# Performance work log

Hardware: AMD Instinct MI355X
Metric: run time of the kernel (lower is better)

The kernel has to match this reference:

```python
import jax, jax.numpy as jnp
import numpy as np

S, N, H, AD, AR = 256, 1024, 512, 128, 2

def setup_inputs() -> dict:
    key = jax.random.key(0)
    k0, k1, k2, k3, k4, k5 = jax.random.split(key, 6)
    xav1 = np.sqrt(2.0 / (H + AD)).astype(np.float32)   # xavier_normal std for [H,AD]
    xav2 = np.sqrt(2.0 / (AD + AR)).astype(np.float32)  # xavier_normal std for [AD,AR]
    return {
        "pre_emb_padded": jax.random.normal(k0, (S, N, H), jnp.float32),
        "fol_emb_padded": jax.random.normal(k1, (S, N, H), jnp.float32),
        "pre_attn_mask": jnp.zeros((N, S), jnp.bool_),
        "fol_attn_mask": jnp.zeros((N, S), jnp.bool_),
        "pre_is_valid": jnp.ones((N,), jnp.int32),
        "fol_is_valid": jnp.ones((N,), jnp.int32),
        "W1_pre": jax.random.normal(k2, (H, AD), jnp.float32) * xav1,
        "W2_pre": jax.random.normal(k3, (AD, AR), jnp.float32) * xav2,
        "W1_fol": jax.random.normal(k4, (H, AD), jnp.float32) * xav1,
        "W2_fol": jax.random.normal(k5, (AD, AR), jnp.float32) * xav2,
    }

def _attn_pool(emb, mask, W1, W2):
    # emb: [S, N, H] -> x: [N, S, H]
    x = jnp.transpose(emb, (1, 0, 2))
    s = jnp.tanh(x @ W1) @ W2                 # [N, S, 2]
    s = jax.nn.softmax(s, axis=1)             # softmax over seq (first softmax)
    s = jnp.transpose(s, (0, 2, 1))           # [N, 2, S]
    s = jnp.where(mask[:, None, :], -jnp.inf, s)
    s = jax.nn.softmax(s, axis=-1)            # masked second softmax over seq
    return jnp.einsum('nrs,nsh->nrh', s, x)   # [N, 2, H]

def _scatter_valid(h, valid):
    # reproduce the python valid-list gather: valid rows take next chunk, else zeros
    pos = jnp.cumsum(valid) - 1               # [N]
    return jnp.where((valid > 0)[:, None, None], h[pos], jnp.zeros((), h.dtype))

def reference(pre_emb_padded, fol_emb_padded, pre_attn_mask, fol_attn_mask,
              pre_is_valid, fol_is_valid, W1_pre, W2_pre, W1_fol, W2_fol):
    h_pre = _scatter_valid(_attn_pool(pre_emb_padded, pre_attn_mask, W1_pre, W2_pre), pre_is_valid)
    h_fol = _scatter_valid(_attn_pool(fol_emb_padded, fol_attn_mask, W1_fol, W2_fol), fol_is_valid)
    # mean over the attn_r=2 rows, concat along feature dim -> [N, 1, 2H]
    return jnp.concatenate([h_pre.mean(axis=1, keepdims=True),
                            h_fol.mean(axis=1, keepdims=True)], axis=2)
```

## Files before the change

### kernel.cpp

```cpp
#include <hip/hip_runtime.h>
#include <hip/hip_bf16.h>
#include <cstdint>
#include <cstddef>

#define S_ 256
#define N_ 1024
#define H_ 512
#define AD_ 128
static constexpr int M_TOTAL = N_ * S_;

typedef __attribute__((ext_vector_type(8))) short short8;
typedef __attribute__((ext_vector_type(4))) float f32x4;

__global__ __launch_bounds__(256) void k_w1frag(
    const float* __restrict__ w1_pre, const float* __restrict__ w1_fol,
    unsigned short* __restrict__ w1f) {
  int idx = blockIdx.x * 256 + threadIdx.x;
  int st = blockIdx.y;
  const float* w1 = st ? w1_fol : w1_pre;
  int j = idx & 7;
  int lane = (idx >> 3) & 63;
  int c = (idx >> 9) & 7;
  int kk = idx >> 12;
  int k = kk * 32 + ((lane >> 4) << 3) + j;
  int d = c * 16 + (lane & 15);
  __hip_bfloat16 hb = __float2bfloat16(w1[(size_t)k * AD_ + d]);
  w1f[(size_t)st * 65536 + idx] = *(unsigned short*)&hb;
}

__global__ __launch_bounds__(1024) void k_scan(
    const int* __restrict__ valid_pre, const int* __restrict__ valid_fol,
    int* __restrict__ pos) {
  const int st = blockIdx.x;
  const int* valid = st ? valid_fol : valid_pre;
  __shared__ int buf[1024];
  const int t = threadIdx.x;
  buf[t] = valid[t];
  __syncthreads();
  for (int off = 1; off < 1024; off <<= 1) {
    int v = (t >= off) ? buf[t - off] : 0;
    __syncthreads();
    buf[t] += v;
    __syncthreads();
  }
  pos[st * N_ + t] = buf[t] - 1;
}

__global__ __launch_bounds__(512) void k_logits(
    const float* __restrict__ emb_pre, const float* __restrict__ emb_fol,
    const unsigned short* __restrict__ w1f,
    const float* __restrict__ w2_pre, const float* __restrict__ w2_fol,
    float* __restrict__ logits) {
  __shared__ __align__(16) unsigned char As[16384];
  __shared__ float part[8][16][2];

  const int bid = blockIdx.x;
  const int st  = bid >> 7;
  const int idx = bid & 127;
  const int nc  = idx >> 1;
  const int sh  = idx & 1;
  const int n0 = nc * 16, s0 = sh * 128;
  const float* __restrict__ emb = st ? emb_fol : emb_pre;
  const float* __restrict__ w2  = st ? w2_fol : w2_pre;

  const int t = threadIdx.x;
  const int w = t >> 6, lane = t & 63;
  const int r16 = lane & 15, kq = lane >> 4;

  short8 B[16];
  {
    const unsigned short* bb = w1f + (size_t)st * 65536 + w * 512 + (size_t)lane * 8;
#pragma unroll
    for (int kk = 0; kk < 16; ++kk) B[kk] = *(const short8*)(bb + kk * 4096);
  }
  const float w2v0 = w2[(w * 16 + r16) * 2 + 0];
  const float w2v1 = w2[(w * 16 + r16) * 2 + 1];

  const int srow = t >> 5;
  const int sl   = t & 31;
  const size_t SSTR = (size_t)N_ * H_;
  const float* sbase = emb + ((size_t)s0 * N_ + n0 + srow) * H_ + sl * 4;
  unsigned wadr[4];
#pragma unroll
  for (int j = 0; j < 4; ++j) {
    int g = j * 16 + (sl >> 1);
    wadr[j] = (unsigned)(srow * 1024 + ((g ^ (srow & 7)) * 16) + (sl & 1) * 8);
  }
  unsigned radr[16];
#pragma unroll
  for (int kk = 0; kk < 16; ++kk)
    radr[kk] = (unsigned)(r16 * 1024 + (((kk * 4 + kq) ^ (r16 & 7)) * 16));

  float4 nxt[4];
#pragma unroll
  for (int j = 0; j < 4; ++j) nxt[j] = *(const float4*)(sbase + j * 128);
#pragma unroll
  for (int j = 0; j < 4; ++j) {
    union { unsigned long long u; __hip_bfloat162 h[2]; } p;
    p.h[0] = __float22bfloat162_rn(make_float2(nxt[j].x, nxt[j].y));
    p.h[1] = __float22bfloat162_rn(make_float2(nxt[j].z, nxt[j].w));
    *(unsigned long long*)&As[wadr[j]] = p.u;
  }
  __syncthreads();

  for (int ss = 0; ss < 128; ++ss) {
    if (ss < 127) {
      const float* nb = sbase + (size_t)(ss + 1) * SSTR;
#pragma unroll
      for (int j = 0; j < 4; ++j) nxt[j] = *(const float4*)(nb + j * 128);
    }

    f32x4 acc = (f32x4){0.f, 0.f, 0.f, 0.f};
#pragma unroll
    for (int kk = 0; kk < 16; ++kk) {
      short8 a = *(const short8*)&As[radr[kk]];
      acc = __builtin_amdgcn_mfma_f32_16x16x32_bf16(a, B[kk], acc, 0, 0, 0);
    }

#pragma unroll
    for (int q = 0; q < 4; ++q) {
      float xc = fminf(fmaxf(acc[q], -10.f), 10.f);
      float e  = __expf(2.f * xc);
      float th = (e - 1.f) / (e + 1.f);
      float p0 = th * w2v0;
      float p1 = th * w2v1;
      p0 += __shfl_xor(p0, 1); p0 += __shfl_xor(p0, 2);
      p0 += __shfl_xor(p0, 4); p0 += __shfl_xor(p0, 8);
      p1 += __shfl_xor(p1, 1); p1 += __shfl_xor(p1, 2);
      p1 += __shfl_xor(p1, 4); p1 += __shfl_xor(p1, 8);
      if (r16 == 0) {
        part[w][kq * 4 + q][0] = p0;
        part[w][kq * 4 + q][1] = p1;
      }
    }
    __syncthreads();

    if (t < 32) {
      int row = t >> 1, rr = t & 1;
      float v = 0.f;
#pragma unroll
      for (int g = 0; g < 8; ++g) v += part[g][row][rr];
      logits[((size_t)st * M_TOTAL + (size_t)(s0 + ss) * N_ + n0 + row) * 2 + rr] = v;
    }
    if (ss < 127) {
#pragma unroll
      for (int j = 0; j < 4; ++j) {
        union { unsigned long long u; __hip_bfloat162 h[2]; } p;
        p.h[0] = __float22bfloat162_rn(make_float2(nxt[j].x, nxt[j].y));
        p.h[1] = __float22bfloat162_rn(make_float2(nxt[j].z, nxt[j].w));
        *(unsigned long long*)&As[wadr[j]] = p.u;
      }
    }
    __syncthreads();
  }
}

template <bool MAXRED>
__device__ __forceinline__ float blockRed(float v, float* buf) {
#pragma unroll
  for (int off = 32; off; off >>= 1) {
    float o = __shfl_xor(v, off);
    v = MAXRED ? fmaxf(v, o) : (v + o);
  }
  __syncthreads();
  if ((threadIdx.x & 63) == 0) buf[threadIdx.x >> 6] = v;
  __syncthreads();
  float r = buf[0];
#pragma unroll
  for (int i = 1; i < 4; ++i) r = MAXRED ? fmaxf(r, buf[i]) : (r + buf[i]);
  return r;
}

__global__ __launch_bounds__(256) void k_softmax(
    const float* __restrict__ logits,
    const unsigned char* __restrict__ mask_pre, const unsigned char* __restrict__ mask_fol,
    float* __restrict__ wbar) {
  const int n  = blockIdx.x;
  const int st = blockIdx.y;
  const unsigned char* mask = st ? mask_fol : mask_pre;
  const int s = threadIdx.x;

  float2 l = *(const float2*)&logits[((size_t)st * M_TOTAL + (size_t)s * N_ + n) * 2];
  const bool mk = mask[(size_t)n * S_ + s] != 0;

  __shared__ float buf[4];
  float q[2];
  float lv[2] = {l.x, l.y};
#pragma unroll
  for (int r = 0; r < 2; ++r) {
    float m1 = blockRed<true>(lv[r], buf);
    float e1 = __expf(lv[r] - m1);
    float s1 = blockRed<false>(e1, buf);
    float p1 = e1 / s1;
    float v  = mk ? -INFINITY : p1;
    float m2 = blockRed<true>(v, buf);
    float e2 = mk ? 0.f : __expf(v - m2);
    float s2 = blockRed<false>(e2, buf);
    q[r] = e2 / s2;
  }
  wbar[((size_t)st * N_ + n) * S_ + s] = 0.5f * (q[0] + q[1]);
}

__global__ __launch_bounds__(512) void k_pv2(
    const float* __restrict__ emb_pre, const float* __restrict__ emb_fol,
    const float* __restrict__ wbar,
    float* __restrict__ part) {
  const int bid = blockIdx.x;
  const int st  = bid >> 7;
  const int idx = bid & 127;
  const int nc  = idx >> 1;
  const int sh  = idx & 1;
  const int n0 = nc * 16, s0 = sh * 128;
  const float* __restrict__ emb = st ? emb_fol : emb_pre;

  const int t = threadIdx.x;
  const int nl = t >> 5;
  const int c0 = (t & 31) * 4;

  __shared__ float wl[16][128];
  for (int i = t; i < 2048; i += 512) {
    int j = i >> 7, sl = i & 127;
    wl[j][sl] = wbar[((size_t)st * N_ + n0 + j) * S_ + s0 + sl];
  }
  __syncthreads();

  float4 acc[4], cur[4], nxt[4];
#pragma unroll
  for (int j = 0; j < 4; ++j) acc[j] = (float4){0.f, 0.f, 0.f, 0.f};

  const float* rowp = emb + ((size_t)(s0 + 127) * N_ + n0 + nl) * H_ + c0;
  const size_t SSTR = (size_t)N_ * H_;
#pragma unroll
  for (int j = 0; j < 4; ++j) cur[j] = *(const float4*)(rowp + j * 128);

  for (int sl = 127; sl >= 0; --sl) {
    const float* nrow = rowp - SSTR;
    if (sl > 0) {
#pragma unroll
      for (int j = 0; j < 4; ++j) nxt[j] = *(const float4*)(nrow + j * 128);
    }
    const float wv = wl[nl][sl];
#pragma unroll
    for (int j = 0; j < 4; ++j) {
      acc[j].x += wv * cur[j].x;
      acc[j].y += wv * cur[j].y;
      acc[j].z += wv * cur[j].z;
      acc[j].w += wv * cur[j].w;
    }
#pragma unroll
    for (int j = 0; j < 4; ++j) cur[j] = nxt[j];
    rowp = nrow;
  }

  float* pp = part + (((size_t)(st * 2 + sh) * N_) + n0 + nl) * H_ + c0;
#pragma unroll
  for (int j = 0; j < 4; ++j) *(float4*)(pp + j * 128) = acc[j];
}

__global__ __launch_bounds__(256) void k_combine(
    const float* __restrict__ part, const int* __restrict__ pos,
    const int* __restrict__ valid_pre, const int* __restrict__ valid_fol,
    float* __restrict__ out) {
  const int n = blockIdx.x, t = threadIdx.x;
  const int st = t >> 7;
  const int c = (t & 127) * 4;
  const int* valid = st ? valid_fol : valid_pre;
  float4 r = {0.f, 0.f, 0.f, 0.f};
  if (valid[n] > 0) {
    int np = pos[st * N_ + n]; if (np < 0) np = 0;
    float4 a = *(const float4*)&part[(((size_t)(st * 2 + 0) * N_) + np) * H_ + c];
    float4 b = *(const float4*)&part[(((size_t)(st * 2 + 1) * N_) + np) * H_ + c];
    r.x = a.x + b.x; r.y = a.y + b.y; r.z = a.z + b.z; r.w = a.w + b.w;
  }
  *(float4*)&out[(size_t)n * 1024 + st * 512 + c] = r;
}

extern "C" void kernel_launch(void* const* d_in, const int* in_sizes, int n_in,
                              void* d_out, int out_size, void* d_ws, size_t ws_size,
                              hipStream_t stream) {
  const float* emb_pre = (const float*)d_in[0];
  const float* emb_fol = (const float*)d_in[1];
  const unsigned char* mask_pre = (const unsigned char*)d_in[2];
  const unsigned char* mask_fol = (const unsigned char*)d_in[3];
  const int* valid_pre = (const int*)d_in[4];
  const int* valid_fol = (const int*)d_in[5];
  const float* w1_pre = (const float*)d_in[6];
  const float* w2_pre = (const float*)d_in[7];
  const float* w1_fol = (const float*)d_in[8];
  const float* w2_fol = (const float*)d_in[9];
  float* out = (float*)d_out;

  char* ws = (char*)d_ws;
  unsigned short* w1f = (unsigned short*)ws;
  int*   pos    = (int*)(ws + 262144);
  float* logits = (float*)(ws + 270336);
  float* wbar   = (float*)(ws + 270336 + 4194304);
  float* part   = (float*)(ws + 270336 + 4194304 + 2097152);

  hipLaunchKernelGGL(k_w1frag, dim3(256, 2), dim3(256), 0, stream,
                     w1_pre, w1_fol, w1f);
  hipLaunchKernelGGL(k_scan, dim3(2), dim3(1024), 0, stream,
                     valid_pre, valid_fol, pos);
  hipLaunchKernelGGL(k_logits, dim3(256), dim3(512), 0, stream,
                     emb_pre, emb_fol, w1f, w2_pre, w2_fol, logits);
  hipLaunchKernelGGL(k_softmax, dim3(N_, 2), dim3(256), 0, stream,
                     logits, mask_pre, mask_fol, wbar);
  hipLaunchKernelGGL(k_pv2, dim3(256), dim3(512), 0, stream,
                     emb_pre, emb_fol, wbar, part);
  hipLaunchKernelGGL(k_combine, dim3(N_), dim3(256), 0, stream,
                     part, pos, valid_pre, valid_fol, out);
}
```

Before: 438.6 us.

## Double-buffer LDS tile and defer logit reduction to cut per-step barriers

The logits kernel now ping-pongs between two LDS A tiles and two partial-sum buffers. That lets each step write the next tile, prefetch the tile after that from global memory, and reduce the previous step's partials, all before the MFMA chain, using a single barrier per iteration instead of two. The MFMA accumulation is split into two independent accumulators to shorten the dependency chain, and the final reduction is spread across all waves. This doubles LDS use per block, which may lower occupancy, and keeps more registers live.

```diff
diff --git a/kernel.cpp b/kernel.cpp
--- a/kernel.cpp
+++ b/kernel.cpp
@@ -51,8 +51,8 @@
     const unsigned short* __restrict__ w1f,
     const float* __restrict__ w2_pre, const float* __restrict__ w2_fol,
     float* __restrict__ logits) {
-  __shared__ __align__(16) unsigned char As[16384];
-  __shared__ float part[8][16][2];
+  __shared__ __align__(16) unsigned char As[32768];
+  __shared__ float part[2][8][16][2];
 
   const int bid = blockIdx.x;
   const int st  = bid >> 7;
@@ -86,10 +86,8 @@
     int g = j * 16 + (sl >> 1);
     wadr[j] = (unsigned)(srow * 1024 + ((g ^ (srow & 7)) * 16) + (sl & 1) * 8);
   }
-  unsigned radr[16];
-#pragma unroll
-  for (int kk = 0; kk < 16; ++kk)
-    radr[kk] = (unsigned)(r16 * 1024 + (((kk * 4 + kq) ^ (r16 & 7)) * 16));
+  const int rrow = w * 2 + ((lane >> 1) & 1);
+  const int rr   = lane & 1;
 
   float4 nxt[4];
 #pragma unroll
@@ -101,25 +99,52 @@
     p.h[1] = __float22bfloat162_rn(make_float2(nxt[j].z, nxt[j].w));
     *(unsigned long long*)&As[wadr[j]] = p.u;
   }
+#pragma unroll
+  for (int j = 0; j < 4; ++j) nxt[j] = *(const float4*)(sbase + SSTR + j * 128);
   __syncthreads();
 
   for (int ss = 0; ss < 128; ++ss) {
+    const int cur = ss & 1;
+    const int nb  = cur ^ 1;
+    const unsigned abase = (unsigned)(cur << 14);
+
     if (ss < 127) {
-      const float* nb = sbase + (size_t)(ss + 1) * SSTR;
-#pragma unroll
-      for (int j = 0; j < 4; ++j) nxt[j] = *(const float4*)(nb + j * 128);
-    }
-
-    f32x4 acc = (f32x4){0.f, 0.f, 0.f, 0.f};
+#pragma unroll
+      for (int j = 0; j < 4; ++j) {
+        union { unsigned long long u; __hip_bfloat162 h[2]; } p;
+        p.h[0] = __float22bfloat162_rn(make_float2(nxt[j].x, nxt[j].y));
+        p.h[1] = __float22bfloat162_rn(make_float2(nxt[j].z, nxt[j].w));
+        *(unsigned long long*)&As[(nb << 14) + wadr[j]] = p.u;
+      }
+    }
+    if (ss < 126) {
+      const float* nbp = sbase + (size_t)(ss + 2) * SSTR;
+#pragma unroll
+      for (int j = 0; j < 4; ++j) nxt[j] = *(const float4*)(nbp + j * 128);
+    }
+    if (ss > 0 && (lane & 63) < 4) {
+      float v = 0.f;
+#pragma unroll
+      for (int g = 0; g < 8; ++g) v += part[nb][g][rrow][rr];
+      logits[((size_t)st * M_TOTAL + (size_t)(s0 + ss - 1) * N_ + n0 + rrow) * 2 + rr] = v;
+    }
+
+    f32x4 acc0 = (f32x4){0.f, 0.f, 0.f, 0.f};
+    f32x4 acc1 = (f32x4){0.f, 0.f, 0.f, 0.f};
 #pragma unroll
     for (int kk = 0; kk < 16; ++kk) {
-      short8 a = *(const short8*)&As[radr[kk]];
-      acc = __builtin_amdgcn_mfma_f32_16x16x32_bf16(a, B[kk], acc, 0, 0, 0);
+      const unsigned ra = abase +
+          (unsigned)(r16 * 1024 + (((kk * 4 + kq) ^ (r16 & 7)) * 16));
+      short8 a = *(const short8*)&As[ra];
+      if (kk & 1)
+        acc1 = __builtin_amdgcn_mfma_f32_16x16x32_bf16(a, B[kk], acc1, 0, 0, 0);
+      else
+        acc0 = __builtin_amdgcn_mfma_f32_16x16x32_bf16(a, B[kk], acc0, 0, 0, 0);
     }
 
 #pragma unroll
     for (int q = 0; q < 4; ++q) {
-      float xc = fminf(fmaxf(acc[q], -10.f), 10.f);
+      float xc = fminf(fmaxf(acc0[q] + acc1[q], -10.f), 10.f);
       float e  = __expf(2.f * xc);
       float th = (e - 1.f) / (e + 1.f);
       float p0 = th * w2v0;
@@ -129,29 +154,18 @@
       p1 += __shfl_xor(p1, 1); p1 += __shfl_xor(p1, 2);
       p1 += __shfl_xor(p1, 4); p1 += __shfl_xor(p1, 8);
       if (r16 == 0) {
-        part[w][kq * 4 + q][0] = p0;
-        part[w][kq * 4 + q][1] = p1;
+        part[cur][w][kq * 4 + q][0] = p0;
+        part[cur][w][kq * 4 + q][1] = p1;
       }
     }
     __syncthreads();
-
-    if (t < 32) {
-      int row = t >> 1, rr = t & 1;
-      float v = 0.f;
-#pragma unroll
-      for (int g = 0; g < 8; ++g) v += part[g][row][rr];
-      logits[((size_t)st * M_TOTAL + (size_t)(s0 + ss) * N_ + n0 + row) * 2 + rr] = v;
-    }
-    if (ss < 127) {
-#pragma unroll
-      for (int j = 0; j < 4; ++j) {
-        union { unsigned long long u; __hip_bfloat162 h[2]; } p;
-        p.h[0] = __float22bfloat162_rn(make_float2(nxt[j].x, nxt[j].y));
-        p.h[1] = __float22bfloat162_rn(make_float2(nxt[j].z, nxt[j].w));
-        *(unsigned long long*)&As[wadr[j]] = p.u;
-      }
-    }
-    __syncthreads();
+  }
+
+  if ((lane & 63) < 4) {
+    float v = 0.f;
+#pragma unroll
+    for (int g = 0; g < 8; ++g) v += part[1][g][rrow][rr];
+    logits[((size_t)st * M_TOTAL + (size_t)(s0 + 127) * N_ + n0 + rrow) * 2 + rr] = v;
   }
 }
 
```

Measured after the change: 438.0 us. About the same (-0.1%).
